# Kernel optimization log

Hardware: AMD Instinct MI355X
Metric: run time of the kernel (lower is better)

Reference implementation:

```python
import jax, jax.numpy as jnp
import numpy as np

NUM_GRAPHS = 128

def setup_inputs() -> dict:
    key = jax.random.key(0)
    k1, k2, k3, k4, k5, k6 = jax.random.split(key, 6)
    N, E, H = 100000, 3200000, 256
    x = jax.random.normal(k1, (N, 1), dtype=jnp.float32)
    edge_index = jax.random.randint(k2, (2, E), 0, N, dtype=jnp.int64)
    batch = jnp.sort(jax.random.randint(k3, (N,), 0, NUM_GRAPHS, dtype=jnp.int64))
    # SAGEConv lin_l: [in=1 -> out=H], plus bias; final Linear [H -> 1]
    W_l = jax.random.normal(k4, (1, H), dtype=jnp.float32) / jnp.sqrt(1.0)
    b_l = jnp.zeros((H,), dtype=jnp.float32)
    W_out = jax.random.normal(k5, (H, 1), dtype=jnp.float32) / jnp.sqrt(H)
    b_out = jax.random.normal(k6, (1,), dtype=jnp.float32) * 0.01
    return {"x": x, "edge_index": edge_index, "batch": batch,
            "W_l": W_l, "b_l": b_l, "W_out": W_out, "b_out": b_out}

def reference(x, edge_index, batch, W_l, b_l, W_out, b_out):
    N = x.shape[0]
    src, dst = edge_index[0], edge_index[1]
    # SAGEConv(aggr='sum', root_weight=False): agg[i] = sum_{j->i} x[j]; out = agg @ W_l + b_l
    agg = jax.ops.segment_sum(x[src], dst, num_segments=N)  # [N,1]
    h = agg @ W_l + b_l                                      # [N,H]
    h = jax.nn.relu(h)
    # global_mean_pool over batch ids
    sums = jax.ops.segment_sum(h, batch, num_segments=NUM_GRAPHS)          # [G,H]
    counts = jax.ops.segment_sum(jnp.ones((N,), h.dtype), batch, num_segments=NUM_GRAPHS)
    pooled = sums / jnp.maximum(counts, 1.0)[:, None]
    out = pooled @ W_out + b_out                             # [G,1]
    return jax.nn.relu(out)
```

## Files before the change

kernel.cpp:

```cpp
#include <hip/hip_runtime.h>


#define GMAX  128
#define HMAX  256
#define BS    256
#define NBMAX 512
#define SG    512
#define CEDGE 6400


__global__ __launch_bounds__(1024) void s1_count(const int* __restrict__ ei,
                                                 unsigned* __restrict__ cnt,
                                                 int E, int NB, int QpB) {
  __shared__ unsigned h[NBMAX];
  int tid = threadIdx.x;
  for (int b = tid; b < NBMAX; b += 1024) h[b] = 0u;
  __syncthreads();
  int Q = E >> 2;
  int q0 = blockIdx.x * QpB;
  int q1 = min(q0 + QpB, Q);
  const int4* d4 = (const int4*)(ei + E);
  for (int q = q0 + tid; q < q1; q += 1024) {
    int4 d = d4[q];
    atomicAdd(&h[d.x >> 8], 1u);
    atomicAdd(&h[d.y >> 8], 1u);
    atomicAdd(&h[d.z >> 8], 1u);
    atomicAdd(&h[d.w >> 8], 1u);
  }
  if (blockIdx.x == 0)
    for (int e = (Q << 2) + tid; e < E; e += 1024)
      atomicAdd(&h[ei[E + e] >> 8], 1u);
  __syncthreads();
  for (int b = tid; b < NB; b += 1024)
    cnt[(size_t)blockIdx.x * NBMAX + b] = h[b];
}

__global__ __launch_bounds__(SG) void s_scan(const unsigned* __restrict__ cnt,
                                             unsigned* __restrict__ off,
                                             unsigned* __restrict__ tot,
                                             float* __restrict__ gsum,
                                             float* __restrict__ gcnt,
                                             unsigned* __restrict__ done) {
  __shared__ unsigned s[SG];
  int b = blockIdx.x, t = threadIdx.x;
  unsigned c = cnt[(size_t)t * NBMAX + b];
  s[t] = c;
  __syncthreads();
  for (int o = 1; o < SG; o <<= 1) {
    unsigned v = (t >= o) ? s[t - o] : 0u;
    __syncthreads();
    s[t] += v;
    __syncthreads();
  }
  off[(size_t)t * NBMAX + b] = s[t] - c;
  if (t == SG - 1) tot[b] = s[t];
  if (b == 0) {
    if (t < GMAX) { gsum[t] = 0.f; gcnt[t] = 0.f; }
    if (t == 0) done[0] = 0u;
  }
}

__global__ __launch_bounds__(1024) void s2_scatter(const int* __restrict__ ei,
                                                   const unsigned* __restrict__ cnt,
                                                   const unsigned* __restrict__ off,
                                                   unsigned* __restrict__ pairs,
                                                   int E, int NB, int QpB, int CAP) {
  __shared__ unsigned lp[CEDGE];
  __shared__ unsigned short lb[CEDGE];
  __shared__ unsigned lbase[NBMAX];
  __shared__ unsigned lrank[NBMAX];
  __shared__ unsigned hb[NBMAX];
  __shared__ unsigned sc[NBMAX];
  int tid = threadIdx.x, blk = blockIdx.x;

  if (tid < NBMAX) {
    unsigned c = (tid < NB) ? cnt[(size_t)blk * NBMAX + tid] : 0u;
    sc[tid] = c;
    lrank[tid] = 0u;
    if (tid < NB)
      hb[tid] = (unsigned)tid * (unsigned)CAP + off[(size_t)blk * NBMAX + tid];
  }
  __syncthreads();
  for (int o = 1; o < NBMAX; o <<= 1) {
    unsigned v = 0u;
    if (tid < NBMAX && tid >= o) v = sc[tid - o];
    __syncthreads();
    if (tid < NBMAX) sc[tid] += v;
    __syncthreads();
  }
  if (tid < NB) {
    unsigned c = cnt[(size_t)blk * NBMAX + tid];
    lbase[tid] = sc[tid] - c;
  }
  __syncthreads();

  int Q = E >> 2;
  int q0 = blk * QpB;
  int q1 = min(q0 + QpB, Q);
  const int4* s4 = (const int4*)ei;
  const int4* d4 = (const int4*)(ei + E);
  for (int q = q0 + tid; q < q1; q += 1024) {
    int4 s = s4[q];
    int4 d = d4[q];
    { int b = d.x >> 8; unsigned r = atomicAdd(&lrank[b], 1u);
      unsigned p = lbase[b] + r;
      lp[p] = ((unsigned)s.x << 8) | (unsigned)(d.x & 255); lb[p] = (unsigned short)b; }
    { int b = d.y >> 8; unsigned r = atomicAdd(&lrank[b], 1u);
      unsigned p = lbase[b] + r;
      lp[p] = ((unsigned)s.y << 8) | (unsigned)(d.y & 255); lb[p] = (unsigned short)b; }
    { int b = d.z >> 8; unsigned r = atomicAdd(&lrank[b], 1u);
      unsigned p = lbase[b] + r;
      lp[p] = ((unsigned)s.z << 8) | (unsigned)(d.z & 255); lb[p] = (unsigned short)b; }
    { int b = d.w >> 8; unsigned r = atomicAdd(&lrank[b], 1u);
      unsigned p = lbase[b] + r;
      lp[p] = ((unsigned)s.w << 8) | (unsigned)(d.w & 255); lb[p] = (unsigned short)b; }
  }
  int total = (q1 - q0) * 4;
  if (blk == 0) {
    for (int e = (Q << 2) + tid; e < E; e += 1024) {
      int d = ei[E + e], s = ei[e];
      int b = d >> 8; unsigned r = atomicAdd(&lrank[b], 1u);
      unsigned p = lbase[b] + r;
      lp[p] = ((unsigned)s << 8) | (unsigned)(d & 255); lb[p] = (unsigned short)b;
    }
    total += (E & 3);
  }
  if (total > CEDGE) total = CEDGE;
  __syncthreads();

  unsigned capu = (unsigned)CAP;
  for (int i = tid; i < total; i += 1024) {
    unsigned b = lb[i];
    unsigned slot = hb[b] + ((unsigned)i - lbase[b]);
    if (slot < (b + 1u) * capu)
      pairs[slot] = lp[i];
  }
}

__global__ __launch_bounds__(1024) void s3_reduce(
    const unsigned* __restrict__ pairs, const unsigned* __restrict__ tot,
    const float* __restrict__ x, const int* __restrict__ batch,
    const float* __restrict__ Wl, const float* __restrict__ bl,
    const float* __restrict__ Wo, const float* __restrict__ b_out,
    float* __restrict__ gsum, float* __restrict__ gcnt,
    unsigned* __restrict__ done, float* __restrict__ out,
    int N, int H, int G, int CAP, int NB) {
  __shared__ float acc[BS];
  __shared__ float sWl[HMAX], sbl[HMAX], sWo[HMAX];
  __shared__ float ls[GMAX], lc[GMAX];
  __shared__ unsigned ticket;
  int tid = threadIdx.x;
  if (tid < H) { sWl[tid] = Wl[tid]; sbl[tid] = bl[tid]; sWo[tid] = Wo[tid]; }
  if (tid < GMAX) { ls[tid] = 0.f; lc[tid] = 0.f; }

  for (int b = blockIdx.x; b < NB; b += gridDim.x) {
    if (tid < BS) acc[tid] = 0.f;
    __syncthreads();

    unsigned lo = (unsigned)b * (unsigned)CAP;
    unsigned cnt = min(tot[b], (unsigned)CAP);
    unsigned q4 = cnt >> 2;
    const uint4* p4 = (const uint4*)(pairs + lo);
    for (unsigned i = tid; i < q4; i += 1024) {
      uint4 p = p4[i];
      atomicAdd(&acc[p.x & 255u], x[p.x >> 8]);
      atomicAdd(&acc[p.y & 255u], x[p.y >> 8]);
      atomicAdd(&acc[p.z & 255u], x[p.z >> 8]);
      atomicAdd(&acc[p.w & 255u], x[p.w >> 8]);
    }
    if (tid < (int)(cnt & 3u)) {
      unsigned p = pairs[lo + (q4 << 2) + tid];
      atomicAdd(&acc[p & 255u], x[p >> 8]);
    }
    __syncthreads();

    int node = b * BS + tid;
    if (tid < BS && node < N) {
      float a = acc[tid], f = 0.f;
#pragma unroll 8
      for (int k = 0; k < H; ++k) {
        float hh = fmaf(a, sWl[k], sbl[k]);
        f = fmaf(fmaxf(hh, 0.f), sWo[k], f);
      }
      int g = batch[node];
      atomicAdd(&ls[g], f);
      atomicAdd(&lc[g], 1.f);
    }
    __syncthreads();
  }

  if (tid < GMAX && lc[tid] != 0.f) {
    atomicAdd(&gsum[tid], ls[tid]);
    atomicAdd(&gcnt[tid], lc[tid]);
  }
  __syncthreads();
  if (tid == 0)
    ticket = __hip_atomic_fetch_add(done, 1u, __ATOMIC_ACQ_REL,
                                    __HIP_MEMORY_SCOPE_AGENT);
  __syncthreads();
  if (ticket == gridDim.x - 1 && tid < G) {
    float s = __hip_atomic_load(&gsum[tid], __ATOMIC_RELAXED, __HIP_MEMORY_SCOPE_AGENT);
    float c = __hip_atomic_load(&gcnt[tid], __ATOMIC_RELAXED, __HIP_MEMORY_SCOPE_AGENT);
    out[tid] = fmaxf(s / fmaxf(c, 1.f) + b_out[0], 0.f);
  }
}


__global__ __launch_bounds__(256) void fb_scatter(const int* __restrict__ ei,
                                                  const float* __restrict__ x,
                                                  float* __restrict__ agg, int E) {
  int t = blockIdx.x * blockDim.x + threadIdx.x;
  if (t < E) atomicAdd(&agg[ei[E + t]], x[ei[t]]);
}

__global__ __launch_bounds__(256) void fb_node(const float* __restrict__ agg,
                                               const int* __restrict__ batch,
                                               const float* __restrict__ Wl,
                                               const float* __restrict__ bl,
                                               const float* __restrict__ Wo,
                                               float* __restrict__ gsum,
                                               float* __restrict__ gcnt, int N, int H) {
  __shared__ float sWl[HMAX], sbl[HMAX], sWo[HMAX];
  __shared__ float ls[GMAX], lc[GMAX];
  int tid = threadIdx.x;
  if (tid < H) { sWl[tid] = Wl[tid]; sbl[tid] = bl[tid]; sWo[tid] = Wo[tid]; }
  if (tid < GMAX) { ls[tid] = 0.f; lc[tid] = 0.f; }
  __syncthreads();
  int i = blockIdx.x * blockDim.x + tid;
  if (i < N) {
    float a = agg[i], f = 0.f;
    for (int k = 0; k < H; ++k) {
      float hh = fmaf(a, sWl[k], sbl[k]);
      f = fmaf(fmaxf(hh, 0.f), sWo[k], f);
    }
    int g = batch[i];
    atomicAdd(&ls[g], f);
    atomicAdd(&lc[g], 1.f);
  }
  __syncthreads();
  if (tid < GMAX && lc[tid] != 0.f) {
    atomicAdd(&gsum[tid], ls[tid]);
    atomicAdd(&gcnt[tid], lc[tid]);
  }
}

__global__ void fb_final(const float* __restrict__ gsum,
                         const float* __restrict__ gcnt,
                         const float* __restrict__ b_out,
                         float* __restrict__ out, int G) {
  int g = blockIdx.x * blockDim.x + threadIdx.x;
  if (g < G) out[g] = fmaxf(gsum[g] / fmaxf(gcnt[g], 1.f) + b_out[0], 0.f);
}


extern "C" void kernel_launch(void* const* d_in, const int* in_sizes, int n_in,
                              void* d_out, int out_size, void* d_ws, size_t ws_size,
                              hipStream_t stream) {
  const float* x     = (const float*)d_in[0];
  const int*   ei    = (const int*)d_in[1];
  const int*   batch = (const int*)d_in[2];
  const float* Wl    = (const float*)d_in[3];
  const float* bl    = (const float*)d_in[4];
  const float* Wo    = (const float*)d_in[5];
  const float* bo    = (const float*)d_in[6];
  float* out = (float*)d_out;

  int N = in_sizes[0];
  int E = in_sizes[1] / 2;
  int H = in_sizes[3];
  int G = out_size;

  int NB = (N + BS - 1) / BS;
  int Q   = E >> 2;
  int QpB = (Q + SG - 1) / SG;

  int avg = (NB > 0) ? E / NB : 0;
  int CAP = (2 * avg + 4095) & ~4095;
  if (CAP < 4096) CAP = 4096;

  const size_t W_MAT = (size_t)SG * NBMAX;
  const size_t HDRW  = 2 * W_MAT + NBMAX + 2 * GMAX + 4;
  size_t need = (HDRW + (size_t)NB * (size_t)CAP) * 4u;

  unsigned* w = (unsigned*)d_ws;
  if (NB <= NBMAX && ws_size >= need && H <= HMAX && G <= GMAX &&
      QpB * 4 + 4 <= CEDGE) {
    unsigned* cnt   = w;
    unsigned* off   = cnt + W_MAT;
    unsigned* tot   = off + W_MAT;
    float*    gsum  = (float*)(tot + NBMAX);
    float*    gcnt  = gsum + GMAX;
    unsigned* done  = (unsigned*)(gcnt + GMAX);
    unsigned* pairs = done + 4;

    s1_count<<<SG, 1024, 0, stream>>>(ei, cnt, E, NB, QpB);
    s_scan<<<NB, SG, 0, stream>>>(cnt, off, tot, gsum, gcnt, done);
    s2_scatter<<<SG, 1024, 0, stream>>>(ei, cnt, off, pairs, E, NB, QpB, CAP);
    s3_reduce<<<256, 1024, 0, stream>>>(pairs, tot, x, batch, Wl, bl, Wo, bo,
                                        gsum, gcnt, done, out, N, H, G, CAP, NB);
  } else {
    float* agg  = (float*)d_ws;
    float* gsum = agg + N;
    float* gcnt = gsum + GMAX;
    hipMemsetAsync(d_ws, 0, ((size_t)N + 2 * GMAX) * 4u, stream);
    fb_scatter<<<(E + 255) / 256, 256, 0, stream>>>(ei, x, agg, E);
    fb_node<<<(N + 255) / 256, 256, 0, stream>>>(agg, batch, Wl, bl, Wo,
                                                 gsum, gcnt, N, H);
    fb_final<<<1, 256, 0, stream>>>(gsum, gcnt, bo, out, G);
  }
}
```

Before: 135.1 us.

## Fuse count and scatter passes using global atomic cursors per bucket

```diff
diff --git a/kernel.cpp b/kernel.cpp
--- a/kernel.cpp
+++ b/kernel.cpp
@@ -9,89 +9,19 @@
 #define CEDGE 6400
 
 
-__global__ __launch_bounds__(1024) void s1_count(const int* __restrict__ ei,
-                                                 unsigned* __restrict__ cnt,
-                                                 int E, int NB, int QpB) {
-  __shared__ unsigned h[NBMAX];
-  int tid = threadIdx.x;
-  for (int b = tid; b < NBMAX; b += 1024) h[b] = 0u;
-  __syncthreads();
-  int Q = E >> 2;
-  int q0 = blockIdx.x * QpB;
-  int q1 = min(q0 + QpB, Q);
-  const int4* d4 = (const int4*)(ei + E);
-  for (int q = q0 + tid; q < q1; q += 1024) {
-    int4 d = d4[q];
-    atomicAdd(&h[d.x >> 8], 1u);
-    atomicAdd(&h[d.y >> 8], 1u);
-    atomicAdd(&h[d.z >> 8], 1u);
-    atomicAdd(&h[d.w >> 8], 1u);
-  }
-  if (blockIdx.x == 0)
-    for (int e = (Q << 2) + tid; e < E; e += 1024)
-      atomicAdd(&h[ei[E + e] >> 8], 1u);
-  __syncthreads();
-  for (int b = tid; b < NB; b += 1024)
-    cnt[(size_t)blockIdx.x * NBMAX + b] = h[b];
-}
-
-__global__ __launch_bounds__(SG) void s_scan(const unsigned* __restrict__ cnt,
-                                             unsigned* __restrict__ off,
-                                             unsigned* __restrict__ tot,
-                                             float* __restrict__ gsum,
-                                             float* __restrict__ gcnt,
-                                             unsigned* __restrict__ done) {
-  __shared__ unsigned s[SG];
-  int b = blockIdx.x, t = threadIdx.x;
-  unsigned c = cnt[(size_t)t * NBMAX + b];
-  s[t] = c;
-  __syncthreads();
-  for (int o = 1; o < SG; o <<= 1) {
-    unsigned v = (t >= o) ? s[t - o] : 0u;
-    __syncthreads();
-    s[t] += v;
-    __syncthreads();
-  }
-  off[(size_t)t * NBMAX + b] = s[t] - c;
-  if (t == SG - 1) tot[b] = s[t];
-  if (b == 0) {
-    if (t < GMAX) { gsum[t] = 0.f; gcnt[t] = 0.f; }
-    if (t == 0) done[0] = 0u;
-  }
-}
-
-__global__ __launch_bounds__(1024) void s2_scatter(const int* __restrict__ ei,
-                                                   const unsigned* __restrict__ cnt,
-                                                   const unsigned* __restrict__ off,
-                                                   unsigned* __restrict__ pairs,
-                                                   int E, int NB, int QpB, int CAP) {
+__global__ __launch_bounds__(1024) void s12_scatter(const int* __restrict__ ei,
+                                                    unsigned* __restrict__ cursor,
+                                                    unsigned* __restrict__ pairs,
+                                                    int E, int NB, int QpB, int CAP) {
   __shared__ unsigned lp[CEDGE];
   __shared__ unsigned short lb[CEDGE];
+  __shared__ unsigned hcnt[NBMAX];
   __shared__ unsigned lbase[NBMAX];
   __shared__ unsigned lrank[NBMAX];
   __shared__ unsigned hb[NBMAX];
-  __shared__ unsigned sc[NBMAX];
   int tid = threadIdx.x, blk = blockIdx.x;
 
-  if (tid < NBMAX) {
-    unsigned c = (tid < NB) ? cnt[(size_t)blk * NBMAX + tid] : 0u;
-    sc[tid] = c;
-    lrank[tid] = 0u;
-    if (tid < NB)
-      hb[tid] = (unsigned)tid * (unsigned)CAP + off[(size_t)blk * NBMAX + tid];
-  }
-  __syncthreads();
-  for (int o = 1; o < NBMAX; o <<= 1) {
-    unsigned v = 0u;
-    if (tid < NBMAX && tid >= o) v = sc[tid - o];
-    __syncthreads();
-    if (tid < NBMAX) sc[tid] += v;
-    __syncthreads();
-  }
-  if (tid < NB) {
-    unsigned c = cnt[(size_t)blk * NBMAX + tid];
-    lbase[tid] = sc[tid] - c;
-  }
+  if (tid < NBMAX) { hcnt[tid] = 0u; lrank[tid] = 0u; }
   __syncthreads();
 
   int Q = E >> 2;
@@ -99,21 +29,58 @@
   int q1 = min(q0 + QpB, Q);
   const int4* s4 = (const int4*)ei;
   const int4* d4 = (const int4*)(ei + E);
+
+  int4 rs[2], rd[2];
+  int nq = 0;
   for (int q = q0 + tid; q < q1; q += 1024) {
-    int4 s = s4[q];
-    int4 d = d4[q];
-    { int b = d.x >> 8; unsigned r = atomicAdd(&lrank[b], 1u);
-      unsigned p = lbase[b] + r;
-      lp[p] = ((unsigned)s.x << 8) | (unsigned)(d.x & 255); lb[p] = (unsigned short)b; }
-    { int b = d.y >> 8; unsigned r = atomicAdd(&lrank[b], 1u);
-      unsigned p = lbase[b] + r;
-      lp[p] = ((unsigned)s.y << 8) | (unsigned)(d.y & 255); lb[p] = (unsigned short)b; }
-    { int b = d.z >> 8; unsigned r = atomicAdd(&lrank[b], 1u);
-      unsigned p = lbase[b] + r;
-      lp[p] = ((unsigned)s.z << 8) | (unsigned)(d.z & 255); lb[p] = (unsigned short)b; }
-    { int b = d.w >> 8; unsigned r = atomicAdd(&lrank[b], 1u);
-      unsigned p = lbase[b] + r;
-      lp[p] = ((unsigned)s.w << 8) | (unsigned)(d.w & 255); lb[p] = (unsigned short)b; }
+    rs[nq] = s4[q];
+    rd[nq] = d4[q];
+    ++nq;
+  }
+  for (int i = 0; i < nq; ++i) {
+    atomicAdd(&hcnt[rd[i].x >> 8], 1u);
+    atomicAdd(&hcnt[rd[i].y >> 8], 1u);
+    atomicAdd(&hcnt[rd[i].z >> 8], 1u);
+    atomicAdd(&hcnt[rd[i].w >> 8], 1u);
+  }
+  if (blk == 0)
+    for (int e = (Q << 2) + tid; e < E; e += 1024)
+      atomicAdd(&hcnt[ei[E + e] >> 8], 1u);
+  __syncthreads();
+
+  unsigned myc = (tid < NBMAX) ? hcnt[tid] : 0u;
+  for (int o = 1; o < NBMAX; o <<= 1) {
+    unsigned v = 0u;
+    if (tid < NBMAX && tid >= o) v = hcnt[tid - o];
+    __syncthreads();
+    if (tid < NBMAX) hcnt[tid] += v;
+    __syncthreads();
+  }
+  if (tid < NBMAX) {
+    lbase[tid] = hcnt[tid] - myc;
+    unsigned rsv = 0u;
+    if (tid < NB && myc) rsv = atomicAdd(&cursor[tid], myc);
+    hb[tid] = (unsigned)tid * (unsigned)CAP + rsv;
+  }
+  __syncthreads();
+
+  for (int i = 0; i < nq; ++i) {
+    { int b = rd[i].x >> 8; unsigned r = atomicAdd(&lrank[b], 1u);
+      unsigned p = lbase[b] + r;
+      lp[p] = ((unsigned)rs[i].x << 8) | (unsigned)(rd[i].x & 255);
+      lb[p] = (unsigned short)b; }
+    { int b = rd[i].y >> 8; unsigned r = atomicAdd(&lrank[b], 1u);
+      unsigned p = lbase[b] + r;
+      lp[p] = ((unsigned)rs[i].y << 8) | (unsigned)(rd[i].y & 255);
+      lb[p] = (unsigned short)b; }
+    { int b = rd[i].z >> 8; unsigned r = atomicAdd(&lrank[b], 1u);
+      unsigned p = lbase[b] + r;
+      lp[p] = ((unsigned)rs[i].z << 8) | (unsigned)(rd[i].z & 255);
+      lb[p] = (unsigned short)b; }
+    { int b = rd[i].w >> 8; unsigned r = atomicAdd(&lrank[b], 1u);
+      unsigned p = lbase[b] + r;
+      lp[p] = ((unsigned)rs[i].w << 8) | (unsigned)(rd[i].w & 255);
+      lb[p] = (unsigned short)b; }
   }
   int total = (q1 - q0) * 4;
   if (blk == 0) {
@@ -121,7 +88,8 @@
       int d = ei[E + e], s = ei[e];
       int b = d >> 8; unsigned r = atomicAdd(&lrank[b], 1u);
       unsigned p = lbase[b] + r;
-      lp[p] = ((unsigned)s << 8) | (unsigned)(d & 255); lb[p] = (unsigned short)b;
+      lp[p] = ((unsigned)s << 8) | (unsigned)(d & 255);
+      lb[p] = (unsigned short)b;
     }
     total += (E & 3);
   }
@@ -138,57 +106,53 @@
 }
 
 __global__ __launch_bounds__(1024) void s3_reduce(
-    const unsigned* __restrict__ pairs, const unsigned* __restrict__ tot,
+    const unsigned* __restrict__ pairs, const unsigned* __restrict__ cursor,
     const float* __restrict__ x, const int* __restrict__ batch,
     const float* __restrict__ Wl, const float* __restrict__ bl,
     const float* __restrict__ Wo, const float* __restrict__ b_out,
     float* __restrict__ gsum, float* __restrict__ gcnt,
     unsigned* __restrict__ done, float* __restrict__ out,
-    int N, int H, int G, int CAP, int NB) {
+    int N, int H, int G, int CAP) {
   __shared__ float acc[BS];
   __shared__ float sWl[HMAX], sbl[HMAX], sWo[HMAX];
   __shared__ float ls[GMAX], lc[GMAX];
   __shared__ unsigned ticket;
-  int tid = threadIdx.x;
+  int tid = threadIdx.x, b = blockIdx.x;
+  if (tid < BS) acc[tid] = 0.f;
   if (tid < H) { sWl[tid] = Wl[tid]; sbl[tid] = bl[tid]; sWo[tid] = Wo[tid]; }
   if (tid < GMAX) { ls[tid] = 0.f; lc[tid] = 0.f; }
-
-  for (int b = blockIdx.x; b < NB; b += gridDim.x) {
-    if (tid < BS) acc[tid] = 0.f;
-    __syncthreads();
-
-    unsigned lo = (unsigned)b * (unsigned)CAP;
-    unsigned cnt = min(tot[b], (unsigned)CAP);
-    unsigned q4 = cnt >> 2;
-    const uint4* p4 = (const uint4*)(pairs + lo);
-    for (unsigned i = tid; i < q4; i += 1024) {
-      uint4 p = p4[i];
-      atomicAdd(&acc[p.x & 255u], x[p.x >> 8]);
-      atomicAdd(&acc[p.y & 255u], x[p.y >> 8]);
-      atomicAdd(&acc[p.z & 255u], x[p.z >> 8]);
-      atomicAdd(&acc[p.w & 255u], x[p.w >> 8]);
+  __syncthreads();
+
+  unsigned lo = (unsigned)b * (unsigned)CAP;
+  unsigned cnt = min(cursor[b], (unsigned)CAP);
+  unsigned q4 = cnt >> 2;
+  const uint4* p4 = (const uint4*)(pairs + lo);
+  for (unsigned i = tid; i < q4; i += 1024) {
+    uint4 p = p4[i];
+    atomicAdd(&acc[p.x & 255u], x[p.x >> 8]);
+    atomicAdd(&acc[p.y & 255u], x[p.y >> 8]);
+    atomicAdd(&acc[p.z & 255u], x[p.z >> 8]);
+    atomicAdd(&acc[p.w & 255u], x[p.w >> 8]);
+  }
+  if (tid < (int)(cnt & 3u)) {
+    unsigned p = pairs[lo + (q4 << 2) + tid];
+    atomicAdd(&acc[p & 255u], x[p >> 8]);
+  }
+  __syncthreads();
+
+  int node = b * BS + tid;
+  if (tid < BS && node < N) {
+    float a = acc[tid], f = 0.f;
+#pragma unroll 8
+    for (int k = 0; k < H; ++k) {
+      float hh = fmaf(a, sWl[k], sbl[k]);
+      f = fmaf(fmaxf(hh, 0.f), sWo[k], f);
     }
-    if (tid < (int)(cnt & 3u)) {
-      unsigned p = pairs[lo + (q4 << 2) + tid];
-      atomicAdd(&acc[p & 255u], x[p >> 8]);
-    }
-    __syncthreads();
-
-    int node = b * BS + tid;
-    if (tid < BS && node < N) {
-      float a = acc[tid], f = 0.f;
-#pragma unroll 8
-      for (int k = 0; k < H; ++k) {
-        float hh = fmaf(a, sWl[k], sbl[k]);
-        f = fmaf(fmaxf(hh, 0.f), sWo[k], f);
-      }
-      int g = batch[node];
-      atomicAdd(&ls[g], f);
-      atomicAdd(&lc[g], 1.f);
-    }
-    __syncthreads();
-  }
-
+    int g = batch[node];
+    atomicAdd(&ls[g], f);
+    atomicAdd(&lc[g], 1.f);
+  }
+  __syncthreads();
   if (tid < GMAX && lc[tid] != 0.f) {
     atomicAdd(&gsum[tid], ls[tid]);
     atomicAdd(&gcnt[tid], lc[tid]);
@@ -278,26 +242,22 @@
   int CAP = (2 * avg + 4095) & ~4095;
   if (CAP < 4096) CAP = 4096;
 
-  const size_t W_MAT = (size_t)SG * NBMAX;
-  const size_t HDRW  = 2 * W_MAT + NBMAX + 2 * GMAX + 4;
+  const size_t HDRW = NBMAX + 2 * GMAX + 4;
   size_t need = (HDRW + (size_t)NB * (size_t)CAP) * 4u;
 
   unsigned* w = (unsigned*)d_ws;
   if (NB <= NBMAX && ws_size >= need && H <= HMAX && G <= GMAX &&
-      QpB * 4 + 4 <= CEDGE) {
-    unsigned* cnt   = w;
-    unsigned* off   = cnt + W_MAT;
-    unsigned* tot   = off + W_MAT;
-    float*    gsum  = (float*)(tot + NBMAX);
-    float*    gcnt  = gsum + GMAX;
-    unsigned* done  = (unsigned*)(gcnt + GMAX);
-    unsigned* pairs = done + 4;
-
-    s1_count<<<SG, 1024, 0, stream>>>(ei, cnt, E, NB, QpB);
-    s_scan<<<NB, SG, 0, stream>>>(cnt, off, tot, gsum, gcnt, done);
-    s2_scatter<<<SG, 1024, 0, stream>>>(ei, cnt, off, pairs, E, NB, QpB, CAP);
-    s3_reduce<<<256, 1024, 0, stream>>>(pairs, tot, x, batch, Wl, bl, Wo, bo,
-                                        gsum, gcnt, done, out, N, H, G, CAP, NB);
+      QpB * 4 + 4 <= CEDGE && QpB <= 2 * 1024) {
+    unsigned* cursor = w;
+    float*    gsum   = (float*)(cursor + NBMAX);
+    float*    gcnt   = gsum + GMAX;
+    unsigned* done   = (unsigned*)(gcnt + GMAX);
+    unsigned* pairs  = done + 4;
+
+    hipMemsetAsync(w, 0, HDRW * 4u, stream);
+    s12_scatter<<<SG, 1024, 0, stream>>>(ei, cursor, pairs, E, NB, QpB, CAP);
+    s3_reduce<<<NB, 1024, 0, stream>>>(pairs, cursor, x, batch, Wl, bl, Wo, bo,
+                                       gsum, gcnt, done, out, N, H, G, CAP);
   } else {
     float* agg  = (float*)d_ws;
     float* gsum = agg + N;
```

New measurement: 150.8 us. 1.12x slower.
